# Optimization experiments

Measured on AMD Instinct MI355X. Metric: run time of the kernel, lower is better.

## Reference

```python
import math
import jax, jax.numpy as jnp
import numpy as np

B, C, HH, WW = 1, 256, 64, 64
NUM_HEADS = 8
GROUPS = 8
EPS = 1e-5


def setup_inputs() -> dict:
    key = jax.random.key(0)
    ks = jax.random.split(key, 5)
    x = jax.random.normal(ks[0], (B, C, HH, WW), dtype=jnp.float32)
    gn_gamma = jnp.ones((C,), dtype=jnp.float32)
    gn_beta = jnp.zeros((C,), dtype=jnp.float32)
    qkv_w = jax.random.normal(ks[1], (3 * C, C), dtype=jnp.float32) / math.sqrt(C)
    qkv_b = jax.random.normal(ks[2], (3 * C,), dtype=jnp.float32) * 0.02
    proj_w = jax.random.normal(ks[3], (C, C), dtype=jnp.float32) / math.sqrt(C)
    proj_b = jax.random.normal(ks[4], (C,), dtype=jnp.float32) * 0.02
    return {"x": x, "gn_gamma": gn_gamma, "gn_beta": gn_beta,
            "qkv_w": qkv_w, "qkv_b": qkv_b, "proj_w": proj_w, "proj_b": proj_b}


def reference(x, gn_gamma, gn_beta, qkv_w, qkv_b, proj_w, proj_b):
    b, c, h, w = x.shape
    t = h * w
    xf = x.reshape(b, c, t)
    # GroupNorm(8, C): normalize over (C/8 channels x T spatial) per group
    xg = xf.reshape(b, GROUPS, (c // GROUPS) * t)
    mean = xg.mean(axis=-1, keepdims=True)
    var = xg.var(axis=-1, keepdims=True)
    xn = ((xg - mean) * jax.lax.rsqrt(var + EPS)).reshape(b, c, t)
    xn = xn * gn_gamma[:, None] + gn_beta[:, None]
    # 1x1 Conv1d C -> 3C is a channel matmul
    qkv = jnp.einsum('oc,bct->bot', qkv_w, xn) + qkv_b[:, None]  # [b, 3C, t]
    nh = NUM_HEADS
    ch = c // nh
    q, k, v = jnp.split(qkv, 3, axis=1)  # each [b, C, t]
    q = q.reshape(b * nh, ch, t)
    k = k.reshape(b * nh, ch, t)
    v = v.reshape(b * nh, ch, t)
    scale = 1.0 / math.sqrt(math.sqrt(ch))
    weight = jnp.einsum('bct,bcs->bts', q * scale, k * scale)  # [b*nh, t, t]
    weight = jax.nn.softmax(weight.astype(jnp.float32), axis=-1).astype(qkv.dtype)
    a = jnp.einsum('bts,bcs->bct', weight, v).reshape(b, c, t)
    hout = jnp.einsum('oc,bct->bot', proj_w, a) + proj_b[:, None]
    return x + hout.reshape(b, c, h, w)
```

## Files before the change

kernel.cpp:

```cpp
#include <hip/hip_runtime.h>
#include <hip/hip_bf16.h>
#include <math.h>

#define C_DIM 256
#define T_DIM 4096
#define NHEADS 8
#define NGROUPS 8
#define NSPLIT 4
#define SRANGE (T_DIM / NSPLIT)
#define NT (SRANGE / 64)

typedef __attribute__((ext_vector_type(8))) short bf16x8;
typedef __attribute__((ext_vector_type(4))) float f32x4;

#if __has_builtin(__builtin_amdgcn_exp2f)
#define EXP2(x) __builtin_amdgcn_exp2f(x)
#else
#define EXP2(x) exp2f(x)
#endif

#define MFMA16(a, b, c) __builtin_amdgcn_mfma_f32_16x16x32_bf16(a, b, c, 0, 0, 0)

#define WS_PSUM 0
#define WS_PSQ  256
#define WS_QT_F   1024
#define WS_KT_F   (WS_QT_F + 524288)
#define WS_VB_F   (WS_KT_F + 524288)
#define WS_WQB_F  (WS_VB_F + 524288)
#define WS_WPB_F  (WS_WQB_F + 98304)
#define WS_OP_F   (WS_WPB_F + 32768)
#define WS_L_F    (WS_OP_F + NSPLIT * 256 * 4096 / 2)

#define QSCALE 0.2550348527f

__device__ __forceinline__ ushort f2bf(float f) {
  union { float f; unsigned u; } v; v.f = f;
  return (ushort)((v.u + 0x7fffu + ((v.u >> 16) & 1u)) >> 16);
}

__device__ __forceinline__ float bf2f(ushort u) {
  union { unsigned u; float f; } v; v.u = ((unsigned)u) << 16;
  return v.f;
}

__device__ __forceinline__ uint pk2(float a, float b) {
  __hip_bfloat162 h = __float22bfloat162_rn(make_float2(a, b));
  union { __hip_bfloat162 h; uint u; } c; c.h = h; return c.u;
}

__global__ __launch_bounds__(256) void prep(const float* __restrict__ x,
                                            const float* __restrict__ wq,
                                            const float* __restrict__ wp,
                                            float* __restrict__ ws,
                                            ushort* __restrict__ wqb,
                                            ushort* __restrict__ wpb) {
  const int i4 = (blockIdx.x * 256 + threadIdx.x) * 4;
  const int n1 = 768 * 256;
  if (i4 < n1) {
    float4 v = *(const float4*)(wq + i4);
    union { ushort us[4]; uint2 u; } pk;
    pk.us[0] = f2bf(v.x); pk.us[1] = f2bf(v.y); pk.us[2] = f2bf(v.z); pk.us[3] = f2bf(v.w);
    *(uint2*)(wqb + i4) = pk.u;
  } else {
    const int j = i4 - n1;
    float4 v = *(const float4*)(wp + j);
    union { ushort us[4]; uint2 u; } pk;
    pk.us[0] = f2bf(v.x); pk.us[1] = f2bf(v.y); pk.us[2] = f2bf(v.z); pk.us[3] = f2bf(v.w);
    *(uint2*)(wpb + j) = pk.u;
  }
  const int g = blockIdx.x >> 5;
  const int bx = blockIdx.x & 31;
  const size_t base = (size_t)g * 131072 + (size_t)bx * 4096;
  float s = 0.f, s2 = 0.f;
  for (int i = threadIdx.x; i < 4096; i += 256) {
    float v = x[base + i];
    s += v;
    s2 += v * v;
  }
#pragma unroll
  for (int mask = 1; mask <= 32; mask <<= 1) {
    s += __shfl_xor(s, mask, 64);
    s2 += __shfl_xor(s2, mask, 64);
  }
  __shared__ float red[8];
  const int wid = threadIdx.x >> 6;
  if ((threadIdx.x & 63) == 0) { red[wid] = s; red[4 + wid] = s2; }
  __syncthreads();
  if (threadIdx.x == 0) {
    ws[WS_PSUM + g * 32 + bx] = red[0] + red[1] + red[2] + red[3];
    ws[WS_PSQ + g * 32 + bx] = red[4] + red[5] + red[6] + red[7];
  }
}

__global__ __launch_bounds__(256) void qkv_mfma(const float* __restrict__ x,
                                                const float* __restrict__ gamma,
                                                const float* __restrict__ beta,
                                                const float* __restrict__ ws,
                                                const ushort* __restrict__ wqb,
                                                const float* __restrict__ bias,
                                                ushort* __restrict__ qt,
                                                ushort* __restrict__ kt,
                                                ushort* __restrict__ vb) {
  const int t0 = blockIdx.x * 16;
  __shared__ ushort A[16 * 256];
  __shared__ float fg[256], fb[256];
  __shared__ float sm_stat[16];
  const int tid = threadIdx.x;
  {
    const int gg = tid >> 5, i = tid & 31;
    float s = ws[WS_PSUM + gg * 32 + i];
    float s2 = ws[WS_PSQ + gg * 32 + i];
#pragma unroll
    for (int mask = 1; mask <= 16; mask <<= 1) {
      s += __shfl_xor(s, mask, 32);
      s2 += __shfl_xor(s2, mask, 32);
    }
    if (i == 0) {
      const float inv_n = 1.0f / 131072.0f;
      float mean = s * inv_n;
      float var = s2 * inv_n - mean * mean;
      sm_stat[gg] = mean;
      sm_stat[8 + gg] = rsqrtf(var + 1e-5f);
    }
  }
  __syncthreads();
  {
    const int c = tid, gg = c >> 5;
    float fgv = gamma[c] * sm_stat[8 + gg];
    fg[c] = fgv; fb[c] = beta[c] - sm_stat[gg] * fgv;
  }
  __syncthreads();
#pragma unroll
  for (int p = 0; p < 4; ++p) {
    const int idx = p * 256 + tid;
    const int c = idx >> 2;
    const int tin = (idx & 3) * 4;
    float4 xv = *(const float4*)(x + (size_t)c * T_DIM + t0 + tin);
    const float fgc = fg[c], fbc = fb[c];
    float xn[4] = {fmaf(xv.x, fgc, fbc), fmaf(xv.y, fgc, fbc),
                   fmaf(xv.z, fgc, fbc), fmaf(xv.w, fgc, fbc)};
#pragma unroll
    for (int i = 0; i < 4; ++i) {
      const int t = tin + i;
      A[t * 256 + (c ^ ((t & 7) << 3))] = f2bf(xn[i]);
    }
  }
  __syncthreads();

  const int w = tid >> 6, lane = tid & 63, l15 = lane & 15, g = lane >> 4;
  const int ob = blockIdx.y * 384 + w * 96;
  f32x4 acc[6] = {};
  const ushort* wrow[6];
#pragma unroll
  for (int j = 0; j < 6; ++j)
    wrow[j] = wqb + (size_t)(ob + j * 16 + l15) * 256;

  bf16x8 bc[6], bn[6];
#pragma unroll
  for (int j = 0; j < 6; ++j) bc[j] = *(const bf16x8*)(wrow[j] + 8 * g);

#pragma unroll
  for (int kk = 0; kk < 8; ++kk) {
    const bf16x8 af = *(const bf16x8*)(&A[l15 * 256 + ((kk * 32 + 8 * g) ^ ((l15 & 7) << 3))]);
    if (kk < 7) {
#pragma unroll
      for (int j = 0; j < 6; ++j) bn[j] = *(const bf16x8*)(wrow[j] + (kk + 1) * 32 + 8 * g);
    }
#pragma unroll
    for (int j = 0; j < 6; ++j)
      acc[j] = MFMA16(af, bc[j], acc[j]);
#pragma unroll
    for (int j = 0; j < 6; ++j) bc[j] = bn[j];
  }

#pragma unroll
  for (int j = 0; j < 6; ++j) {
    const int o = ob + j * 16 + l15;
    const float bo = bias[o];
    const int tb = t0 + 4 * g;
    if (o < 256) {
      const int hh = o >> 5, d = o & 31;
#pragma unroll
      for (int r = 0; r < 4; ++r)
        qt[((size_t)hh * T_DIM + tb + r) * 32 + d] = f2bf((acc[j][r] + bo) * QSCALE);
    } else if (o < 512) {
      const int oo = o - 256;
      const int hh = oo >> 5, d = oo & 31;
#pragma unroll
      for (int r = 0; r < 4; ++r)
        kt[((size_t)hh * T_DIM + tb + r) * 32 + d] = f2bf(acc[j][r] + bo);
    } else {
      union { ushort us[4]; uint2 u; } pk;
#pragma unroll
      for (int r = 0; r < 4; ++r) pk.us[r] = f2bf(acc[j][r] + bo);
      *(uint2*)(vb + (size_t)(o - 512) * T_DIM + tb) = pk.u;
    }
  }
}

__global__ __launch_bounds__(512, 4) void attn_fwd(const ushort* __restrict__ qt,
                                                   const ushort* __restrict__ kt,
                                                   const ushort* __restrict__ vb,
                                                   ushort* __restrict__ Op,
                                                   float* __restrict__ Lb) {
  const int bid = blockIdx.x;
  const int h = bid & 7;
  const int inner = bid >> 3;
  const int qb = inner & 15;
  const int z = inner >> 4;
  const int tid = threadIdx.x;
  const int w = tid >> 6, lane = tid & 63, l15 = lane & 15, g = lane >> 4;

  __shared__ ushort Klds[2][64 * 40];
  __shared__ ushort Vlds[2][32 * 72];

  const int t_a = qb * 256 + w * 16 + l15;
  const int t_b = t_a + 128;
  const bf16x8 qfa = *(const bf16x8*)(qt + ((size_t)(h * T_DIM + t_a) * 32 + 8 * g));
  const bf16x8 qfb = *(const bf16x8*)(qt + ((size_t)(h * T_DIM + t_b) * 32 + 8 * g));

  f32x4 Oa0 = {}, Oa1 = {}, Ob0 = {}, Ob1 = {};
  float la = 0.f, lb = 0.f;

  const int sbeg = z * SRANGE;
  const int p_row = tid >> 3;
  const int q5 = p_row & 31;
  const int sm_row = (p_row & 32) + 16 * ((q5 >> 2) & 1) + 4 * (q5 >> 3) + (q5 & 3);
  const ushort* kgp = kt + (size_t)h * T_DIM * 32 + (size_t)(sbeg + p_row) * 32 + (tid & 7) * 4;
  const ushort* vgp = vb + (size_t)(h * 32 + (tid >> 4)) * T_DIM + sbeg + (tid & 15) * 4;
  ushort* kw0 = &Klds[0][sm_row * 40 + (tid & 7) * 4];
  ushort* vw0 = &Vlds[0][(tid >> 4) * 72 + (tid & 15) * 4];
  {
    *(uint2*)kw0 = *(const uint2*)kgp;
    *(uint2*)vw0 = *(const uint2*)vgp;
  }
  uint2 kn = *(const uint2*)(kgp + 2048);
  uint2 vn = *(const uint2*)(vgp + 64);
  __syncthreads();

  int cur = 0;
  for (int t = 0; t < NT; ++t) {
    if (t + 1 < NT) {
      *(uint2*)(kw0 + (cur ^ 1) * (64 * 40)) = kn;
      *(uint2*)(vw0 + (cur ^ 1) * (32 * 72)) = vn;
      if (t + 2 < NT) {
        kn = *(const uint2*)(kgp + (size_t)(t + 2) * 2048);
        vn = *(const uint2*)(vgp + (t + 2) * 64);
      }
    }

    const ushort* kbase = &Klds[cur][0];
    const ushort* vbase = &Vlds[cur][0];
    const f32x4 z4 = {};
    const bf16x8 kf0 = *(const bf16x8*)(kbase + (0 * 16 + l15) * 40 + 8 * g);
    const bf16x8 kf1 = *(const bf16x8*)(kbase + (1 * 16 + l15) * 40 + 8 * g);
    const bf16x8 kf2 = *(const bf16x8*)(kbase + (2 * 16 + l15) * 40 + 8 * g);
    const bf16x8 kf3 = *(const bf16x8*)(kbase + (3 * 16 + l15) * 40 + 8 * g);
    __builtin_amdgcn_s_setprio(1);
    f32x4 sa0 = MFMA16(kf0, qfa, z4);
    f32x4 sa1 = MFMA16(kf1, qfa, z4);
    f32x4 sa2 = MFMA16(kf2, qfa, z4);
    f32x4 sa3 = MFMA16(kf3, qfa, z4);
    f32x4 sb0 = MFMA16(kf0, qfb, z4);
    f32x4 sb1 = MFMA16(kf1, qfb, z4);
    f32x4 sb2 = MFMA16(kf2, qfb, z4);
    f32x4 sb3 = MFMA16(kf3, qfb, z4);
    __builtin_amdgcn_s_setprio(0);

    const bf16x8 vf00 = *(const bf16x8*)(vbase + (l15) * 72 + 8 * g);
    const bf16x8 vf01 = *(const bf16x8*)(vbase + (l15) * 72 + 32 + 8 * g);
    const bf16x8 vf10 = *(const bf16x8*)(vbase + (16 + l15) * 72 + 8 * g);
    const bf16x8 vf11 = *(const bf16x8*)(vbase + (16 + l15) * 72 + 32 + 8 * g);

    union { uint u[4]; bf16x8 v; } fa0, fa1, fb0, fb1;
    {
      float p0, p1, p2, p3, p4, p5, p6, p7;
      p0 = EXP2(sa0[0]); p1 = EXP2(sa0[1]); p2 = EXP2(sa0[2]); p3 = EXP2(sa0[3]);
      p4 = EXP2(sa1[0]); p5 = EXP2(sa1[1]); p6 = EXP2(sa1[2]); p7 = EXP2(sa1[3]);
      la += ((p0 + p1) + (p2 + p3)) + ((p4 + p5) + (p6 + p7));
      fa0.u[0] = pk2(p0, p1); fa0.u[1] = pk2(p2, p3);
      fa0.u[2] = pk2(p4, p5); fa0.u[3] = pk2(p6, p7);
      p0 = EXP2(sa2[0]); p1 = EXP2(sa2[1]); p2 = EXP2(sa2[2]); p3 = EXP2(sa2[3]);
      p4 = EXP2(sa3[0]); p5 = EXP2(sa3[1]); p6 = EXP2(sa3[2]); p7 = EXP2(sa3[3]);
      la += ((p0 + p1) + (p2 + p3)) + ((p4 + p5) + (p6 + p7));
      fa1.u[0] = pk2(p0, p1); fa1.u[1] = pk2(p2, p3);
      fa1.u[2] = pk2(p4, p5); fa1.u[3] = pk2(p6, p7);
    }

    __builtin_amdgcn_s_setprio(1);
    Oa0 = MFMA16(vf00, fa0.v, Oa0);
    Oa0 = MFMA16(vf01, fa1.v, Oa0);
    Oa1 = MFMA16(vf10, fa0.v, Oa1);
    Oa1 = MFMA16(vf11, fa1.v, Oa1);
    __builtin_amdgcn_s_setprio(0);

    {
      float p0, p1, p2, p3, p4, p5, p6, p7;
      p0 = EXP2(sb0[0]); p1 = EXP2(sb0[1]); p2 = EXP2(sb0[2]); p3 = EXP2(sb0[3]);
      p4 = EXP2(sb1[0]); p5 = EXP2(sb1[1]); p6 = EXP2(sb1[2]); p7 = EXP2(sb1[3]);
      lb += ((p0 + p1) + (p2 + p3)) + ((p4 + p5) + (p6 + p7));
      fb0.u[0] = pk2(p0, p1); fb0.u[1] = pk2(p2, p3);
      fb0.u[2] = pk2(p4, p5); fb0.u[3] = pk2(p6, p7);
      p0 = EXP2(sb2[0]); p1 = EXP2(sb2[1]); p2 = EXP2(sb2[2]); p3 = EXP2(sb2[3]);
      p4 = EXP2(sb3[0]); p5 = EXP2(sb3[1]); p6 = EXP2(sb3[2]); p7 = EXP2(sb3[3]);
      lb += ((p0 + p1) + (p2 + p3)) + ((p4 + p5) + (p6 + p7));
      fb1.u[0] = pk2(p0, p1); fb1.u[1] = pk2(p2, p3);
      fb1.u[2] = pk2(p4, p5); fb1.u[3] = pk2(p6, p7);
    }

    __builtin_amdgcn_s_setprio(1);
    Ob0 = MFMA16(vf00, fb0.v, Ob0);
    Ob0 = MFMA16(vf01, fb1.v, Ob0);
    Ob1 = MFMA16(vf10, fb0.v, Ob1);
    Ob1 = MFMA16(vf11, fb1.v, Ob1);
    __builtin_amdgcn_s_setprio(0);

    __syncthreads();
    cur ^= 1;
  }

  ushort* opz = Op + (size_t)(z * NHEADS + h) * 32 * T_DIM;
#pragma unroll
  for (int r = 0; r < 4; ++r) {
    const int d0 = 4 * g + r;
    opz[(size_t)d0 * T_DIM + t_a]        = f2bf(Oa0[r]);
    opz[(size_t)(16 + d0) * T_DIM + t_a] = f2bf(Oa1[r]);
    opz[(size_t)d0 * T_DIM + t_b]        = f2bf(Ob0[r]);
    opz[(size_t)(16 + d0) * T_DIM + t_b] = f2bf(Ob1[r]);
  }
  la += __shfl_xor(la, 16, 64);
  la += __shfl_xor(la, 32, 64);
  lb += __shfl_xor(lb, 16, 64);
  lb += __shfl_xor(lb, 32, 64);
  if (g == 0) {
    Lb[(size_t)(z * NHEADS + h) * T_DIM + t_a] = la;
    Lb[(size_t)(z * NHEADS + h) * T_DIM + t_b] = lb;
  }
}

__global__ __launch_bounds__(256) void proj_mfma(const ushort* __restrict__ Op,
                                                 const float* __restrict__ Lb,
                                                 const ushort* __restrict__ wpb,
                                                 const float* __restrict__ bias,
                                                 const float* __restrict__ x,
                                                 float* __restrict__ out) {
  const int t0 = blockIdx.x * 16;
  __shared__ ushort A[16 * 256];
  __shared__ float rinv[128];
  const int tid = threadIdx.x;
  if (tid < 128) {
    const int h = tid >> 4, tt = tid & 15;
    float l = 0.f;
#pragma unroll
    for (int zz = 0; zz < NSPLIT; ++zz)
      l += Lb[(size_t)(zz * NHEADS + h) * T_DIM + t0 + tt];
    rinv[tid] = 1.0f / l;
  }
  __syncthreads();
#pragma unroll
  for (int pass = 0; pass < 4; ++pass) {
    const int c = pass * 64 + (tid >> 2);
    const int h = c >> 5;
    const int tin = (tid & 3) * 4;
    float a4[4] = {0.f, 0.f, 0.f, 0.f};
#pragma unroll
    for (int zz = 0; zz < NSPLIT; ++zz) {
      uint2 v = *(const uint2*)(Op + (size_t)(zz * 256 + c) * T_DIM + t0 + tin);
      const ushort* us = (const ushort*)&v;
#pragma unroll
      for (int i = 0; i < 4; ++i) a4[i] += bf2f(us[i]);
    }
#pragma unroll
    for (int i = 0; i < 4; ++i) {
      const int t = tin + i;
      A[t * 256 + (c ^ ((t & 7) << 3))] = f2bf(a4[i] * rinv[(h << 4) | t]);
    }
  }
  __syncthreads();

  const int w = tid >> 6, lane = tid & 63, l15 = lane & 15, g = lane >> 4;
  const int o0 = blockIdx.y * 128 + w * 32;
  f32x4 acc[2] = {};
  const ushort* wrow[2];
#pragma unroll
  for (int j = 0; j < 2; ++j)
    wrow[j] = wpb + (size_t)(o0 + 16 * j + l15) * 256;

#pragma unroll
  for (int kk = 0; kk < 8; ++kk) {
    const bf16x8 af = *(const bf16x8*)(&A[l15 * 256 + ((kk * 32 + 8 * g) ^ ((l15 & 7) << 3))]);
#pragma unroll
    for (int j = 0; j < 2; ++j) {
      const bf16x8 bfr = *(const bf16x8*)(wrow[j] + kk * 32 + 8 * g);
      acc[j] = MFMA16(af, bfr, acc[j]);
    }
  }

#pragma unroll
  for (int j = 0; j < 2; ++j) {
    const int o = o0 + 16 * j + l15;
    const float bo = bias[o];
    const size_t base = (size_t)o * T_DIM + t0 + 4 * g;
    const float4 xr = *(const float4*)(x + base);
    float4 ov;
    ov.x = acc[j][0] + bo + xr.x;
    ov.y = acc[j][1] + bo + xr.y;
    ov.z = acc[j][2] + bo + xr.z;
    ov.w = acc[j][3] + bo + xr.w;
    *(float4*)(out + base) = ov;
  }
}

extern "C" void kernel_launch(void* const* d_in, const int* in_sizes, int n_in,
                              void* d_out, int out_size, void* d_ws, size_t ws_size,
                              hipStream_t stream) {
  const float* x      = (const float*)d_in[0];
  const float* gamma  = (const float*)d_in[1];
  const float* beta   = (const float*)d_in[2];
  const float* qkv_w  = (const float*)d_in[3];
  const float* qkv_b  = (const float*)d_in[4];
  const float* proj_w = (const float*)d_in[5];
  const float* proj_b = (const float*)d_in[6];
  float* out = (float*)d_out;
  float* ws  = (float*)d_ws;

  ushort* qt  = (ushort*)(ws + WS_QT_F);
  ushort* kt  = (ushort*)(ws + WS_KT_F);
  ushort* vb  = (ushort*)(ws + WS_VB_F);
  ushort* wqb = (ushort*)(ws + WS_WQB_F);
  ushort* wpb = (ushort*)(ws + WS_WPB_F);
  ushort* Op  = (ushort*)(ws + WS_OP_F);
  float*  Lb  = ws + WS_L_F;

  prep<<<256, 256, 0, stream>>>(x, qkv_w, proj_w, ws, wqb, wpb);
  qkv_mfma<<<dim3(256, 2), 256, 0, stream>>>(x, gamma, beta, ws, wqb, qkv_b, qt, kt, vb);
  attn_fwd<<<NHEADS * 16 * NSPLIT, 512, 0, stream>>>(qt, kt, vb, Op, Lb);
  proj_mfma<<<dim3(256, 2), 256, 0, stream>>>(Op, Lb, wpb, proj_b, x, out);
}
```

Baseline: 67.59 us.

## Split QKV by q/k/v slab with LDS-staged stores; halve attention block size

The QKV projection grid grows to three output slabs per time tile, one each for q, k and v. For q and k, results are staged through shared memory so each thread writes coalesced 32-byte rows in place of scattered 2-byte stores. The attention kernel drops from 512 to 256 threads per block with 128 queries per block, doubling the block count, and its K/V tile loads widen to 16-byte vectors. The aim is better store coalescing and more blocks for latency hiding, at the cost of an extra LDS round trip and barriers in the QKV kernel and less K/V tile reuse per block.

Result: no change. 68.05 us (+0.7%).

```diff
diff --git a/kernel.cpp b/kernel.cpp
--- a/kernel.cpp
+++ b/kernel.cpp
@@ -102,6 +102,7 @@
                                                 ushort* __restrict__ kt,
                                                 ushort* __restrict__ vb) {
   const int t0 = blockIdx.x * 16;
+  const int oc = blockIdx.y;
   __shared__ ushort A[16 * 256];
   __shared__ float fg[256], fb[256];
   __shared__ float sm_stat[16];
@@ -148,57 +149,69 @@
   __syncthreads();
 
   const int w = tid >> 6, lane = tid & 63, l15 = lane & 15, g = lane >> 4;
-  const int ob = blockIdx.y * 384 + w * 96;
-  f32x4 acc[6] = {};
-  const ushort* wrow[6];
-#pragma unroll
-  for (int j = 0; j < 6; ++j)
-    wrow[j] = wqb + (size_t)(ob + j * 16 + l15) * 256;
-
-  bf16x8 bc[6], bn[6];
-#pragma unroll
-  for (int j = 0; j < 6; ++j) bc[j] = *(const bf16x8*)(wrow[j] + 8 * g);
+  const int o_loc = w * 64;
+  f32x4 acc[4] = {};
+  const ushort* wrow[4];
+#pragma unroll
+  for (int j = 0; j < 4; ++j)
+    wrow[j] = wqb + (size_t)(oc * 256 + o_loc + j * 16 + l15) * 256;
+
+  bf16x8 bc[4], bn[4];
+#pragma unroll
+  for (int j = 0; j < 4; ++j) bc[j] = *(const bf16x8*)(wrow[j] + 8 * g);
 
 #pragma unroll
   for (int kk = 0; kk < 8; ++kk) {
     const bf16x8 af = *(const bf16x8*)(&A[l15 * 256 + ((kk * 32 + 8 * g) ^ ((l15 & 7) << 3))]);
     if (kk < 7) {
 #pragma unroll
-      for (int j = 0; j < 6; ++j) bn[j] = *(const bf16x8*)(wrow[j] + (kk + 1) * 32 + 8 * g);
-    }
-#pragma unroll
-    for (int j = 0; j < 6; ++j)
+      for (int j = 0; j < 4; ++j) bn[j] = *(const bf16x8*)(wrow[j] + (kk + 1) * 32 + 8 * g);
+    }
+#pragma unroll
+    for (int j = 0; j < 4; ++j)
       acc[j] = MFMA16(af, bc[j], acc[j]);
 #pragma unroll
-    for (int j = 0; j < 6; ++j) bc[j] = bn[j];
-  }
-
-#pragma unroll
-  for (int j = 0; j < 6; ++j) {
-    const int o = ob + j * 16 + l15;
-    const float bo = bias[o];
-    const int tb = t0 + 4 * g;
-    if (o < 256) {
-      const int hh = o >> 5, d = o & 31;
-#pragma unroll
-      for (int r = 0; r < 4; ++r)
-        qt[((size_t)hh * T_DIM + tb + r) * 32 + d] = f2bf((acc[j][r] + bo) * QSCALE);
-    } else if (o < 512) {
-      const int oo = o - 256;
-      const int hh = oo >> 5, d = oo & 31;
-#pragma unroll
-      for (int r = 0; r < 4; ++r)
-        kt[((size_t)hh * T_DIM + tb + r) * 32 + d] = f2bf(acc[j][r] + bo);
-    } else {
+    for (int j = 0; j < 4; ++j) bc[j] = bn[j];
+  }
+
+  if (oc == 2) {
+#pragma unroll
+    for (int j = 0; j < 4; ++j) {
+      const int o = o_loc + j * 16 + l15;
+      const float bo = bias[512 + o];
       union { ushort us[4]; uint2 u; } pk;
 #pragma unroll
       for (int r = 0; r < 4; ++r) pk.us[r] = f2bf(acc[j][r] + bo);
-      *(uint2*)(vb + (size_t)(o - 512) * T_DIM + tb) = pk.u;
-    }
-  }
-}
-
-__global__ __launch_bounds__(512, 4) void attn_fwd(const ushort* __restrict__ qt,
+      *(uint2*)(vb + (size_t)o * T_DIM + t0 + 4 * g) = pk.u;
+    }
+  } else {
+    const float scale = (oc == 0) ? QSCALE : 1.0f;
+    __syncthreads();
+#pragma unroll
+    for (int j = 0; j < 4; ++j) {
+      const int o = o_loc + j * 16 + l15;
+      const float bo = bias[oc * 256 + o];
+#pragma unroll
+      for (int r = 0; r < 4; ++r) {
+        const int t = 4 * g + r;
+        A[t * 256 + (o ^ ((t & 7) << 3))] = f2bf((acc[j][r] + bo) * scale);
+      }
+    }
+    __syncthreads();
+    ushort* dst = (oc == 0) ? qt : kt;
+    const int hh = tid >> 5;
+    const int tt = (tid >> 1) & 15;
+    const int d0 = (tid & 1) * 16;
+    const int sw = (tt & 7) << 3;
+    uint4 v0 = *(uint4*)&A[tt * 256 + ((hh * 32 + d0) ^ sw)];
+    uint4 v1 = *(uint4*)&A[tt * 256 + ((hh * 32 + d0 + 8) ^ sw)];
+    ushort* gp = dst + ((size_t)hh * T_DIM + t0 + tt) * 32 + d0;
+    *(uint4*)gp = v0;
+    *(uint4*)(gp + 8) = v1;
+  }
+}
+
+__global__ __launch_bounds__(256, 4) void attn_fwd(const ushort* __restrict__ qt,
                                                    const ushort* __restrict__ kt,
                                                    const ushort* __restrict__ vb,
                                                    ushort* __restrict__ Op,
@@ -206,16 +219,16 @@
   const int bid = blockIdx.x;
   const int h = bid & 7;
   const int inner = bid >> 3;
-  const int qb = inner & 15;
-  const int z = inner >> 4;
+  const int qb = inner & 31;
+  const int z = inner >> 5;
   const int tid = threadIdx.x;
   const int w = tid >> 6, lane = tid & 63, l15 = lane & 15, g = lane >> 4;
 
   __shared__ ushort Klds[2][64 * 40];
   __shared__ ushort Vlds[2][32 * 72];
 
-  const int t_a = qb * 256 + w * 16 + l15;
-  const int t_b = t_a + 128;
+  const int t_a = qb * 128 + w * 16 + l15;
+  const int t_b = t_a + 64;
   const bf16x8 qfa = *(const bf16x8*)(qt + ((size_t)(h * T_DIM + t_a) * 32 + 8 * g));
   const bf16x8 qfb = *(const bf16x8*)(qt + ((size_t)(h * T_DIM + t_b) * 32 + 8 * g));
 
@@ -223,29 +236,29 @@
   float la = 0.f, lb = 0.f;
 
   const int sbeg = z * SRANGE;
-  const int p_row = tid >> 3;
+  const int p_row = tid >> 2;
   const int q5 = p_row & 31;
   const int sm_row = (p_row & 32) + 16 * ((q5 >> 2) & 1) + 4 * (q5 >> 3) + (q5 & 3);
-  const ushort* kgp = kt + (size_t)h * T_DIM * 32 + (size_t)(sbeg + p_row) * 32 + (tid & 7) * 4;
-  const ushort* vgp = vb + (size_t)(h * 32 + (tid >> 4)) * T_DIM + sbeg + (tid & 15) * 4;
-  ushort* kw0 = &Klds[0][sm_row * 40 + (tid & 7) * 4];
-  ushort* vw0 = &Vlds[0][(tid >> 4) * 72 + (tid & 15) * 4];
+  const ushort* kgp = kt + (size_t)h * T_DIM * 32 + (size_t)(sbeg + p_row) * 32 + (tid & 3) * 8;
+  const ushort* vgp = vb + (size_t)(h * 32 + (tid >> 3)) * T_DIM + sbeg + (tid & 7) * 8;
+  ushort* kw0 = &Klds[0][sm_row * 40 + (tid & 3) * 8];
+  ushort* vw0 = &Vlds[0][(tid >> 3) * 72 + (tid & 7) * 8];
   {
-    *(uint2*)kw0 = *(const uint2*)kgp;
-    *(uint2*)vw0 = *(const uint2*)vgp;
-  }
-  uint2 kn = *(const uint2*)(kgp + 2048);
-  uint2 vn = *(const uint2*)(vgp + 64);
+    *(uint4*)kw0 = *(const uint4*)kgp;
+    *(uint4*)vw0 = *(const uint4*)vgp;
+  }
+  uint4 kn = *(const uint4*)(kgp + 2048);
+  uint4 vn = *(const uint4*)(vgp + 64);
   __syncthreads();
 
   int cur = 0;
   for (int t = 0; t < NT; ++t) {
     if (t + 1 < NT) {
-      *(uint2*)(kw0 + (cur ^ 1) * (64 * 40)) = kn;
-      *(uint2*)(vw0 + (cur ^ 1) * (32 * 72)) = vn;
+      *(uint4*)(kw0 + (cur ^ 1) * (64 * 40)) = kn;
+      *(uint4*)(vw0 + (cur ^ 1) * (32 * 72)) = vn;
       if (t + 2 < NT) {
-        kn = *(const uint2*)(kgp + (size_t)(t + 2) * 2048);
-        vn = *(const uint2*)(vgp + (t + 2) * 64);
+        kn = *(const uint4*)(kgp + (size_t)(t + 2) * 2048);
+        vn = *(const uint4*)(vgp + (t + 2) * 64);
       }
     }
 
@@ -433,7 +446,7 @@
   float*  Lb  = ws + WS_L_F;
 
   prep<<<256, 256, 0, stream>>>(x, qkv_w, proj_w, ws, wqb, wpb);
-  qkv_mfma<<<dim3(256, 2), 256, 0, stream>>>(x, gamma, beta, ws, wqb, qkv_b, qt, kt, vb);
-  attn_fwd<<<NHEADS * 16 * NSPLIT, 512, 0, stream>>>(qt, kt, vb, Op, Lb);
+  qkv_mfma<<<dim3(256, 3), 256, 0, stream>>>(x, gamma, beta, ws, wqb, qkv_b, qt, kt, vb);
+  attn_fwd<<<NHEADS * 32 * NSPLIT, 256, 0, stream>>>(qt, kt, vb, Op, Lb);
   proj_mfma<<<dim3(256, 2), 256, 0, stream>>>(Op, Lb, wpb, proj_b, x, out);
 }
```
